# Kernel tuning notes

Hardware: AMD Instinct MI355X
Metric: run time of the kernel (lower is better)

Reference implementation:

```python
import jax, jax.numpy as jnp
import numpy as np

V, E, H = 50000, 256, 256
B, T = 64, 512


def setup_inputs() -> dict:
    key = jax.random.key(0)
    ks = jax.random.split(key, 6)
    inp = jax.random.randint(ks[0], (B, T), 0, V)
    r = 0.05
    emb = jax.random.uniform(ks[1], (V, E), jnp.float32, -r, r)
    emb = emb.at[0].set(0.0)  # padding_idx=0
    W_ih = jax.random.uniform(ks[2], (3 * H, E), jnp.float32, -r, r)
    W_hh = jax.random.uniform(ks[3], (3 * H, H), jnp.float32, -r, r)
    b_ih = jax.random.uniform(ks[4], (3 * H,), jnp.float32, -r, r)
    b_hh = jax.random.uniform(ks[5], (3 * H,), jnp.float32, -r, r)
    return {"input": inp, "embedding": emb, "W_ih": W_ih, "W_hh": W_hh,
            "b_ih": b_ih, "b_hh": b_hh}


def reference(input, embedding, W_ih, W_hh, b_ih, b_hh):
    # embedded: [T, B, E]
    embedded = embedding[input].transpose(1, 0, 2)
    # batch all input projections in one big GEMM: [T, B, 3H]
    x_proj = jnp.einsum('tbe,ge->tbg', embedded, W_ih) + b_ih
    h0 = jnp.zeros((input.shape[0], W_hh.shape[1]), embedding.dtype)

    def step(h, xp):
        hp = h @ W_hh.T + b_hh                    # [B, 3H]
        xr, xz, xn = jnp.split(xp, 3, axis=-1)
        hr, hz, hn = jnp.split(hp, 3, axis=-1)
        r = jax.nn.sigmoid(xr + hr)
        z = jax.nn.sigmoid(xz + hz)
        n = jnp.tanh(xn + r * hn)
        h_new = (1.0 - z) * n + z * h
        return h_new, h_new

    h_last, outputs = jax.lax.scan(step, h0, x_proj)
    # outputs: [T, B, H]; hidden: [n_layers=1, B, H]
    return outputs, h_last[None, :, :]
```

## Files before the change

### kernel.cpp

```cpp
#include <hip/hip_runtime.h>
#include <hip/hip_bf16.h>


#define T_SEQ 512
#define B_SZ 64
#define E_DIM 256
#define H_DIM 256
#define G3 768

typedef _Float16 half2v __attribute__((ext_vector_type(2)));

#if __has_builtin(__builtin_amdgcn_fdot2)
#define FDOT2(a, b, c) __builtin_amdgcn_fdot2((a), (b), (c), false)
#else
#define FDOT2(a, b, c) ((c) + (float)(a).x * (float)(b).x + (float)(a).y * (float)(b).y)
#endif

#define BM 64
#define BN 64
#define BK 32
#define LDSPAD 4

__global__ __launch_bounds__(256) void xproj_kernel(
    const int* __restrict__ input,
    const float* __restrict__ emb,
    const float* __restrict__ W_ih,
    const float* __restrict__ b_ih,
    float* __restrict__ xp)
{
    __shared__ float As[BM][BK + LDSPAD];
    __shared__ float Bs[BN][BK + LDSPAD];
    __shared__ int rowidx[BM];

    const int tid = threadIdx.x;
    const int m0 = blockIdx.x * BM;
    const int n0 = blockIdx.y * BN;

    if (tid < BM) {
        int m = m0 + tid;
        int t = m >> 6;
        int b = m & 63;
        rowidx[tid] = input[b * T_SEQ + t];
    }
    __syncthreads();

    float acc[4][4] = {};
    const int ty = tid >> 4;
    const int tx = tid & 15;

    for (int k0 = 0; k0 < E_DIM; k0 += BK) {
        #pragma unroll
        for (int i = 0; i < 2; ++i) {
            int f4 = tid * 2 + i;
            int row = f4 >> 3;
            int c4  = (f4 & 7) * 4;
            float4 v = *reinterpret_cast<const float4*>(
                emb + (size_t)rowidx[row] * E_DIM + k0 + c4);
            *reinterpret_cast<float4*>(&As[row][c4]) = v;
        }
        #pragma unroll
        for (int i = 0; i < 2; ++i) {
            int f4 = tid * 2 + i;
            int row = f4 >> 3;
            int c4  = (f4 & 7) * 4;
            float4 v = *reinterpret_cast<const float4*>(
                W_ih + (size_t)(n0 + row) * E_DIM + k0 + c4);
            *reinterpret_cast<float4*>(&Bs[row][c4]) = v;
        }
        __syncthreads();

        #pragma unroll
        for (int kk = 0; kk < BK; kk += 4) {
            float4 a[4], b[4];
            #pragma unroll
            for (int i = 0; i < 4; ++i)
                a[i] = *reinterpret_cast<const float4*>(&As[ty * 4 + i][kk]);
            #pragma unroll
            for (int j = 0; j < 4; ++j)
                b[j] = *reinterpret_cast<const float4*>(&Bs[tx * 4 + j][kk]);
            #pragma unroll
            for (int i = 0; i < 4; ++i)
                #pragma unroll
                for (int j = 0; j < 4; ++j)
                    acc[i][j] += a[i].x * b[j].x + a[i].y * b[j].y +
                                 a[i].z * b[j].z + a[i].w * b[j].w;
        }
        __syncthreads();
    }

    #pragma unroll
    for (int i = 0; i < 4; ++i) {
        int m = m0 + ty * 4 + i;
        int n = n0 + tx * 4;
        float4 o;
        o.x = acc[i][0] + b_ih[n + 0];
        o.y = acc[i][1] + b_ih[n + 1];
        o.z = acc[i][2] + b_ih[n + 2];
        o.w = acc[i][3] + b_ih[n + 3];
        *reinterpret_cast<float4*>(&xp[(size_t)m * G3 + n]) = o;
    }
}

__device__ __forceinline__ float fast_sigmoid(float x) {
    float e = __expf(-x);
    return __builtin_amdgcn_rcpf(1.0f + e);
}
__device__ __forceinline__ float fast_tanh(float x) {
    x = fminf(x, 8.0f);
    float e = __expf(2.0f * x);
    return (e - 1.0f) * __builtin_amdgcn_rcpf(e + 1.0f);
}

__global__ __launch_bounds__(512, 2) void gru_scan_kernel(
    const float* __restrict__ xp,
    const float* __restrict__ W_hh,
    const float* __restrict__ b_hh,
    float* __restrict__ out)
{
    const int b   = blockIdx.x;
    const int tid = threadIdx.x;
    const int jj  = tid >> 2;
    const int q   = tid & 3;

    __shared__ __align__(16) _Float16 hs[2][H_DIM];

    half2v w[6][32];
    #pragma unroll
    for (int s = 0; s < 6; ++s) {
        const float* wr = W_hh + (size_t)(jj + 128 * s) * H_DIM + q * 64;
        #pragma unroll
        for (int i8 = 0; i8 < 8; ++i8) {
            const int src = ((i8 + 2 * q) & 7) * 8;
            float4 f0 = *reinterpret_cast<const float4*>(wr + src);
            float4 f1 = *reinterpret_cast<const float4*>(wr + src + 4);
            w[s][i8 * 4 + 0] = half2v{(_Float16)f0.x, (_Float16)f0.y};
            w[s][i8 * 4 + 1] = half2v{(_Float16)f0.z, (_Float16)f0.w};
            w[s][i8 * 4 + 2] = half2v{(_Float16)f1.x, (_Float16)f1.y};
            w[s][i8 * 4 + 3] = half2v{(_Float16)f1.z, (_Float16)f1.w};
        }
    }
    float bias[6];
    #pragma unroll
    for (int s = 0; s < 6; ++s) bias[s] = b_hh[jj + 128 * s];

    if (tid < 32) reinterpret_cast<uint4*>(hs[0])[tid] = uint4{0, 0, 0, 0};
    __syncthreads();

    const int c0 = jj, c1 = jj + 128;
    float h0 = 0.0f, h1 = 0.0f;

    for (int t = 0; t < T_SEQ; ++t) {
        const float* xrow = xp + ((size_t)t * B_SZ + b) * G3;
        const float xr0 = xrow[c0],       xr1 = xrow[c1];
        const float xz0 = xrow[256 + c0], xz1 = xrow[256 + c1];
        const float xn0 = xrow[512 + c0], xn1 = xrow[512 + c1];

        const uint4* hb = reinterpret_cast<const uint4*>(&hs[t & 1][q * 64]);
        float a0 = 0.f, a1 = 0.f, a2 = 0.f, a3 = 0.f, a4 = 0.f, a5 = 0.f;
        #pragma unroll
        for (int i8 = 0; i8 < 8; ++i8) {
            const uint4 hv = hb[(i8 + 2 * q) & 7];
            const half2v p0 = __builtin_bit_cast(half2v, hv.x);
            const half2v p1 = __builtin_bit_cast(half2v, hv.y);
            const half2v p2 = __builtin_bit_cast(half2v, hv.z);
            const half2v p3 = __builtin_bit_cast(half2v, hv.w);
            a0 = FDOT2(w[0][i8*4+0], p0, a0); a0 = FDOT2(w[0][i8*4+1], p1, a0);
            a0 = FDOT2(w[0][i8*4+2], p2, a0); a0 = FDOT2(w[0][i8*4+3], p3, a0);
            a1 = FDOT2(w[1][i8*4+0], p0, a1); a1 = FDOT2(w[1][i8*4+1], p1, a1);
            a1 = FDOT2(w[1][i8*4+2], p2, a1); a1 = FDOT2(w[1][i8*4+3], p3, a1);
            a2 = FDOT2(w[2][i8*4+0], p0, a2); a2 = FDOT2(w[2][i8*4+1], p1, a2);
            a2 = FDOT2(w[2][i8*4+2], p2, a2); a2 = FDOT2(w[2][i8*4+3], p3, a2);
            a3 = FDOT2(w[3][i8*4+0], p0, a3); a3 = FDOT2(w[3][i8*4+1], p1, a3);
            a3 = FDOT2(w[3][i8*4+2], p2, a3); a3 = FDOT2(w[3][i8*4+3], p3, a3);
            a4 = FDOT2(w[4][i8*4+0], p0, a4); a4 = FDOT2(w[4][i8*4+1], p1, a4);
            a4 = FDOT2(w[4][i8*4+2], p2, a4); a4 = FDOT2(w[4][i8*4+3], p3, a4);
            a5 = FDOT2(w[5][i8*4+0], p0, a5); a5 = FDOT2(w[5][i8*4+1], p1, a5);
            a5 = FDOT2(w[5][i8*4+2], p2, a5); a5 = FDOT2(w[5][i8*4+3], p3, a5);
        }

        a0 += __shfl_xor(a0, 1); a0 += __shfl_xor(a0, 2);
        a1 += __shfl_xor(a1, 1); a1 += __shfl_xor(a1, 2);
        a2 += __shfl_xor(a2, 1); a2 += __shfl_xor(a2, 2);
        a3 += __shfl_xor(a3, 1); a3 += __shfl_xor(a3, 2);
        a4 += __shfl_xor(a4, 1); a4 += __shfl_xor(a4, 2);
        a5 += __shfl_xor(a5, 1); a5 += __shfl_xor(a5, 2);

        const float hr0 = a0 + bias[0], hr1 = a1 + bias[1];
        const float hz0 = a2 + bias[2], hz1 = a3 + bias[3];
        const float hn0 = a4 + bias[4], hn1 = a5 + bias[5];

        const float r0 = fast_sigmoid(xr0 + hr0);
        const float r1 = fast_sigmoid(xr1 + hr1);
        const float z0 = fast_sigmoid(xz0 + hz0);
        const float z1 = fast_sigmoid(xz1 + hz1);
        const float n0 = fast_tanh(xn0 + r0 * hn0);
        const float n1 = fast_tanh(xn1 + r1 * hn1);
        h0 = (1.0f - z0) * n0 + z0 * h0;
        h1 = (1.0f - z1) * n1 + z1 * h1;

        if (q == 0) {
            float* orow = out + ((size_t)t * B_SZ + b) * H_DIM;
            orow[c0] = h0;
            orow[c1] = h1;
            hs[(t + 1) & 1][c0] = (_Float16)h0;
            hs[(t + 1) & 1][c1] = (_Float16)h1;
        }
        __syncthreads();
    }

    if (q == 0) {
        float* hl = out + (size_t)T_SEQ * B_SZ * H_DIM + (size_t)b * H_DIM;
        hl[c0] = h0;
        hl[c1] = h1;
    }
}

extern "C" void kernel_launch(void* const* d_in, const int* in_sizes, int n_in,
                              void* d_out, int out_size, void* d_ws, size_t ws_size,
                              hipStream_t stream) {
    const int*   input = (const int*)d_in[0];
    const float* emb   = (const float*)d_in[1];
    const float* W_ih  = (const float*)d_in[2];
    const float* W_hh  = (const float*)d_in[3];
    const float* b_ih  = (const float*)d_in[4];
    const float* b_hh  = (const float*)d_in[5];
    float* out = (float*)d_out;

    float* xp = (float*)d_ws;

    dim3 gridA(T_SEQ * B_SZ / BM, G3 / BN);
    xproj_kernel<<<gridA, 256, 0, stream>>>(input, emb, W_ih, b_ih, xp);

    gru_scan_kernel<<<B_SZ, 512, 0, stream>>>(xp, W_hh, b_hh, out);
}
```

Baseline: 988.7 us.

## Split GRU scan hidden dot products across 8 lanes with 1024 threads; fold r/z biases

The recurrent scan kernel now uses 1024 threads per block, with each hidden pair handled by 8 lanes instead of 4. This halves the per-thread dot-product chain and the register-held W_hh slice to 96 packed halves. The chain is meant to be the serial critical path of every timestep. In exchange, each step adds an extra shuffle-reduction stage and a larger block barrier. The r and z recurrent biases are also folded into the input-projection epilogue, which removes per-step bias adds.

```diff
diff --git a/kernel.cpp b/kernel.cpp
--- a/kernel.cpp
+++ b/kernel.cpp
@@ -26,6 +26,7 @@
     const float* __restrict__ emb,
     const float* __restrict__ W_ih,
     const float* __restrict__ b_ih,
+    const float* __restrict__ b_hh,
     float* __restrict__ xp)
 {
     __shared__ float As[BM][BK + LDSPAD];
@@ -88,15 +89,16 @@
         __syncthreads();
     }
 
+    const bool foldbh = (n0 < 512);
     #pragma unroll
     for (int i = 0; i < 4; ++i) {
         int m = m0 + ty * 4 + i;
         int n = n0 + tx * 4;
         float4 o;
-        o.x = acc[i][0] + b_ih[n + 0];
-        o.y = acc[i][1] + b_ih[n + 1];
-        o.z = acc[i][2] + b_ih[n + 2];
-        o.w = acc[i][3] + b_ih[n + 3];
+        o.x = acc[i][0] + b_ih[n + 0] + (foldbh ? b_hh[n + 0] : 0.0f);
+        o.y = acc[i][1] + b_ih[n + 1] + (foldbh ? b_hh[n + 1] : 0.0f);
+        o.z = acc[i][2] + b_ih[n + 2] + (foldbh ? b_hh[n + 2] : 0.0f);
+        o.w = acc[i][3] + b_ih[n + 3] + (foldbh ? b_hh[n + 3] : 0.0f);
         *reinterpret_cast<float4*>(&xp[(size_t)m * G3 + n]) = o;
     }
 }
@@ -111,7 +113,9 @@
     return (e - 1.0f) * __builtin_amdgcn_rcpf(e + 1.0f);
 }
 
-__global__ __launch_bounds__(512, 2) void gru_scan_kernel(
+__global__ __attribute__((amdgpu_flat_work_group_size(1024, 1024),
+                          amdgpu_waves_per_eu(4, 4)))
+void gru_scan_kernel(
     const float* __restrict__ xp,
     const float* __restrict__ W_hh,
     const float* __restrict__ b_hh,
@@ -119,35 +123,41 @@
 {
     const int b   = blockIdx.x;
     const int tid = threadIdx.x;
-    const int jj  = tid >> 2;
-    const int q   = tid & 3;
+    const int jj  = tid >> 3;
+    const int q   = tid & 7;
+    const int rot = (q >> 1) & 3;
 
     __shared__ __align__(16) _Float16 hs[2][H_DIM];
 
-    half2v w[6][32];
+    uint32_t w[96];
     #pragma unroll
-    for (int s = 0; s < 6; ++s) {
-        const float* wr = W_hh + (size_t)(jj + 128 * s) * H_DIM + q * 64;
-        #pragma unroll
-        for (int i8 = 0; i8 < 8; ++i8) {
-            const int src = ((i8 + 2 * q) & 7) * 8;
-            float4 f0 = *reinterpret_cast<const float4*>(wr + src);
-            float4 f1 = *reinterpret_cast<const float4*>(wr + src + 4);
-            w[s][i8 * 4 + 0] = half2v{(_Float16)f0.x, (_Float16)f0.y};
-            w[s][i8 * 4 + 1] = half2v{(_Float16)f0.z, (_Float16)f0.w};
-            w[s][i8 * 4 + 2] = half2v{(_Float16)f1.x, (_Float16)f1.y};
-            w[s][i8 * 4 + 3] = half2v{(_Float16)f1.z, (_Float16)f1.w};
-        }
-    }
-    float bias[6];
+    for (int c = 0; c < 4; ++c) {
+        const int cc = (c + rot) & 3;
+        #pragma unroll
+        for (int s = 0; s < 6; ++s) {
+            const float* wr = W_hh + (size_t)(jj + 128 * s) * H_DIM + q * 32 + cc * 8;
+            float4 f0 = *reinterpret_cast<const float4*>(wr);
+            float4 f1 = *reinterpret_cast<const float4*>(wr + 4);
+            w[(c*6+s)*4+0] = __builtin_bit_cast(uint32_t, half2v{(_Float16)f0.x, (_Float16)f0.y});
+            w[(c*6+s)*4+1] = __builtin_bit_cast(uint32_t, half2v{(_Float16)f0.z, (_Float16)f0.w});
+            w[(c*6+s)*4+2] = __builtin_bit_cast(uint32_t, half2v{(_Float16)f1.x, (_Float16)f1.y});
+            w[(c*6+s)*4+3] = __builtin_bit_cast(uint32_t, half2v{(_Float16)f1.z, (_Float16)f1.w});
+        }
+    }
     #pragma unroll
-    for (int s = 0; s < 6; ++s) bias[s] = b_hh[jj + 128 * s];
+    for (int i = 0; i < 96; ++i)
+        asm volatile("" : "+v"(w[i]));
+
+    const float bn0 = b_hh[512 + jj];
+    const float bn1 = b_hh[512 + jj + 128];
 
     if (tid < 32) reinterpret_cast<uint4*>(hs[0])[tid] = uint4{0, 0, 0, 0};
     __syncthreads();
 
     const int c0 = jj, c1 = jj + 128;
     float h0 = 0.0f, h1 = 0.0f;
+
+    #define WH(i) __builtin_bit_cast(half2v, w[i])
 
     for (int t = 0; t < T_SEQ; ++t) {
         const float* xrow = xp + ((size_t)t * B_SZ + b) * G3;
@@ -155,46 +165,44 @@
         const float xz0 = xrow[256 + c0], xz1 = xrow[256 + c1];
         const float xn0 = xrow[512 + c0], xn1 = xrow[512 + c1];
 
-        const uint4* hb = reinterpret_cast<const uint4*>(&hs[t & 1][q * 64]);
         float a0 = 0.f, a1 = 0.f, a2 = 0.f, a3 = 0.f, a4 = 0.f, a5 = 0.f;
-        #pragma unroll
-        for (int i8 = 0; i8 < 8; ++i8) {
-            const uint4 hv = hb[(i8 + 2 * q) & 7];
+        const char* hbase = reinterpret_cast<const char*>(&hs[t & 1][0]) + q * 64;
+        #pragma unroll
+        for (int c = 0; c < 4; ++c) {
+            const int cc = (c + rot) & 3;
+            const uint4 hv = *reinterpret_cast<const uint4*>(hbase + cc * 16);
             const half2v p0 = __builtin_bit_cast(half2v, hv.x);
             const half2v p1 = __builtin_bit_cast(half2v, hv.y);
             const half2v p2 = __builtin_bit_cast(half2v, hv.z);
             const half2v p3 = __builtin_bit_cast(half2v, hv.w);
-            a0 = FDOT2(w[0][i8*4+0], p0, a0); a0 = FDOT2(w[0][i8*4+1], p1, a0);
-            a0 = FDOT2(w[0][i8*4+2], p2, a0); a0 = FDOT2(w[0][i8*4+3], p3, a0);
-            a1 = FDOT2(w[1][i8*4+0], p0, a1); a1 = FDOT2(w[1][i8*4+1], p1, a1);
-            a1 = FDOT2(w[1][i8*4+2], p2, a1); a1 = FDOT2(w[1][i8*4+3], p3, a1);
-            a2 = FDOT2(w[2][i8*4+0], p0, a2); a2 = FDOT2(w[2][i8*4+1], p1, a2);
-            a2 = FDOT2(w[2][i8*4+2], p2, a2); a2 = FDOT2(w[2][i8*4+3], p3, a2);
-            a3 = FDOT2(w[3][i8*4+0], p0, a3); a3 = FDOT2(w[3][i8*4+1], p1, a3);
-            a3 = FDOT2(w[3][i8*4+2], p2, a3); a3 = FDOT2(w[3][i8*4+3], p3, a3);
-            a4 = FDOT2(w[4][i8*4+0], p0, a4); a4 = FDOT2(w[4][i8*4+1], p1, a4);
-            a4 = FDOT2(w[4][i8*4+2], p2, a4); a4 = FDOT2(w[4][i8*4+3], p3, a4);
-            a5 = FDOT2(w[5][i8*4+0], p0, a5); a5 = FDOT2(w[5][i8*4+1], p1, a5);
-            a5 = FDOT2(w[5][i8*4+2], p2, a5); a5 = FDOT2(w[5][i8*4+3], p3, a5);
-        }
-
-        a0 += __shfl_xor(a0, 1); a0 += __shfl_xor(a0, 2);
-        a1 += __shfl_xor(a1, 1); a1 += __shfl_xor(a1, 2);
-        a2 += __shfl_xor(a2, 1); a2 += __shfl_xor(a2, 2);
-        a3 += __shfl_xor(a3, 1); a3 += __shfl_xor(a3, 2);
-        a4 += __shfl_xor(a4, 1); a4 += __shfl_xor(a4, 2);
-        a5 += __shfl_xor(a5, 1); a5 += __shfl_xor(a5, 2);
-
-        const float hr0 = a0 + bias[0], hr1 = a1 + bias[1];
-        const float hz0 = a2 + bias[2], hz1 = a3 + bias[3];
-        const float hn0 = a4 + bias[4], hn1 = a5 + bias[5];
-
-        const float r0 = fast_sigmoid(xr0 + hr0);
-        const float r1 = fast_sigmoid(xr1 + hr1);
-        const float z0 = fast_sigmoid(xz0 + hz0);
-        const float z1 = fast_sigmoid(xz1 + hz1);
-        const float n0 = fast_tanh(xn0 + r0 * hn0);
-        const float n1 = fast_tanh(xn1 + r1 * hn1);
+            const int base = c * 24;
+            a0 = FDOT2(WH(base+ 0), p0, a0); a0 = FDOT2(WH(base+ 1), p1, a0);
+            a0 = FDOT2(WH(base+ 2), p2, a0); a0 = FDOT2(WH(base+ 3), p3, a0);
+            a1 = FDOT2(WH(base+ 4), p0, a1); a1 = FDOT2(WH(base+ 5), p1, a1);
+            a1 = FDOT2(WH(base+ 6), p2, a1); a1 = FDOT2(WH(base+ 7), p3, a1);
+            a2 = FDOT2(WH(base+ 8), p0, a2); a2 = FDOT2(WH(base+ 9), p1, a2);
+            a2 = FDOT2(WH(base+10), p2, a2); a2 = FDOT2(WH(base+11), p3, a2);
+            a3 = FDOT2(WH(base+12), p0, a3); a3 = FDOT2(WH(base+13), p1, a3);
+            a3 = FDOT2(WH(base+14), p2, a3); a3 = FDOT2(WH(base+15), p3, a3);
+            a4 = FDOT2(WH(base+16), p0, a4); a4 = FDOT2(WH(base+17), p1, a4);
+            a4 = FDOT2(WH(base+18), p2, a4); a4 = FDOT2(WH(base+19), p3, a4);
+            a5 = FDOT2(WH(base+20), p0, a5); a5 = FDOT2(WH(base+21), p1, a5);
+            a5 = FDOT2(WH(base+22), p2, a5); a5 = FDOT2(WH(base+23), p3, a5);
+        }
+
+        a0 += __shfl_xor(a0, 1); a0 += __shfl_xor(a0, 2); a0 += __shfl_xor(a0, 4);
+        a1 += __shfl_xor(a1, 1); a1 += __shfl_xor(a1, 2); a1 += __shfl_xor(a1, 4);
+        a2 += __shfl_xor(a2, 1); a2 += __shfl_xor(a2, 2); a2 += __shfl_xor(a2, 4);
+        a3 += __shfl_xor(a3, 1); a3 += __shfl_xor(a3, 2); a3 += __shfl_xor(a3, 4);
+        a4 += __shfl_xor(a4, 1); a4 += __shfl_xor(a4, 2); a4 += __shfl_xor(a4, 4);
+        a5 += __shfl_xor(a5, 1); a5 += __shfl_xor(a5, 2); a5 += __shfl_xor(a5, 4);
+
+        const float r0 = fast_sigmoid(xr0 + a0);
+        const float r1 = fast_sigmoid(xr1 + a1);
+        const float z0 = fast_sigmoid(xz0 + a2);
+        const float z1 = fast_sigmoid(xz1 + a3);
+        const float n0 = fast_tanh(xn0 + r0 * (a4 + bn0));
+        const float n1 = fast_tanh(xn1 + r1 * (a5 + bn1));
         h0 = (1.0f - z0) * n0 + z0 * h0;
         h1 = (1.0f - z1) * n1 + z1 * h1;
 
@@ -213,6 +221,7 @@
         hl[c0] = h0;
         hl[c1] = h1;
     }
+    #undef WH
 }
 
 extern "C" void kernel_launch(void* const* d_in, const int* in_sizes, int n_in,
@@ -229,7 +238,7 @@
     float* xp = (float*)d_ws;
 
     dim3 gridA(T_SEQ * B_SZ / BM, G3 / BN);
-    xproj_kernel<<<gridA, 256, 0, stream>>>(input, emb, W_ih, b_ih, xp);
-
-    gru_scan_kernel<<<B_SZ, 512, 0, stream>>>(xp, W_hh, b_hh, out);
-}
+    xproj_kernel<<<gridA, 256, 0, stream>>>(input, emb, W_ih, b_ih, b_hh, xp);
+
+    gru_scan_kernel<<<B_SZ, 1024, 0, stream>>>(xp, W_hh, b_hh, out);
+}
```

Result: slower. 1.534 ms (+55.1%).
